# Kernel tuning notes

Measured on AMD Instinct MI355X. Metric: run time of the kernel, lower is better.

Reference implementation:

```python
import jax, jax.numpy as jnp
import numpy as np

K = 3  # kernel size along the folded height sub-dimension

def setup_inputs() -> dict:
    key = jax.random.key(0)
    k1, k2 = jax.random.split(key)
    x = jax.random.normal(k1, (1, 48, 56, 56), dtype=jnp.float32)
    W = jax.random.normal(k2, (192, 48, 3), dtype=jnp.float32)
    return {"x": x, "W": W}

def reference(x, W):
    # x: (1,48,56,56) -> (1,48,8,7,56): split H=56 into (8,7)
    t = x.reshape(1, 48, 8, 7, 56)
    # unfold((3,1), padding=(1,0)) acting on the size-7 axis:
    # pad by 1 on each side, then gather K=3 shifted views.
    tp = jnp.pad(t, ((0, 0), (0, 0), (0, 0), (1, 1), (0, 0)))  # (1,48,8,9,56)
    # patches[l,j,n,k,o,m] = tp[l,j,n,o+k,m], o in [0,7), k in [0,3)
    patches = jnp.stack([tp[:, :, :, k:k + 7, :] for k in range(K)], axis=3)  # (1,48,8,3,7,56)
    # einsum 'ljnkom, ijk -> linom' with W (192,48,3)
    out = jnp.einsum('ljnkom,ijk->linom', patches, W)  # (1,192,8,7,56)
    return out.reshape(1, 192, 56, 56)
```

## Files before the change

kernel.cpp:

```cpp
#include <hip/hip_runtime.h>


#define CH_IN 48
#define CH_OUT 192
#define HW 56
#define SP 3136
#define OB 7
#define M4 14
#define COLS 112
#define SEGS 16
#define JSEG (CH_IN / SEGS)
#define BCOL 16
#define CG 7

__device__ __forceinline__ void fma4(float4& a, float s, const float4& b) {
    a.x += s * b.x; a.y += s * b.y; a.z += s * b.z; a.w += s * b.w;
}
__device__ __forceinline__ void add4(float4& a, const float4& b) {
    a.x += b.x; a.y += b.y; a.z += b.z; a.w += b.w;
}

__global__ __launch_bounds__(256) void conv_split16_kernel(const float* __restrict__ x,
                                                           const float* __restrict__ W,
                                                           float* __restrict__ out) {
    __shared__ float4 lds[SEGS][OB][BCOL];

    const int c   = threadIdx.x & (BCOL - 1);
    const int seg = threadIdx.x >> 4;
    const int i   = blockIdx.x / CG;
    const int cg  = blockIdx.x % CG;

    const int col = cg * BCOL + c;
    const int n   = col / M4;
    const int m4  = col % M4;

    const float* xcol = x + seg * (JSEG * SP) + n * (OB * HW) + m4 * 4;
    const float* wrow = W + i * (CH_IN * 3) + seg * (JSEG * 3);

    float4 acc[OB];
#pragma unroll
    for (int o = 0; o < OB; ++o) acc[o] = make_float4(0.f, 0.f, 0.f, 0.f);

#pragma unroll
    for (int j = 0; j < JSEG; ++j) {
        const float w0 = wrow[j * 3 + 0];
        const float w1 = wrow[j * 3 + 1];
        const float w2 = wrow[j * 3 + 2];

        const float* xj = xcol + j * SP;
        float4 xv[OB];
#pragma unroll
        for (int o = 0; o < OB; ++o)
            xv[o] = *reinterpret_cast<const float4*>(xj + o * HW);

#pragma unroll
        for (int o = 0; o < OB; ++o) {
            if (o > 0)      fma4(acc[o], w0, xv[o - 1]);
            fma4(acc[o], w1, xv[o]);
            if (o < OB - 1) fma4(acc[o], w2, xv[o + 1]);
        }
    }

#pragma unroll
    for (int o = 0; o < OB; ++o) lds[seg][o][c] = acc[o];
    __syncthreads();

    const int t = threadIdx.x;
    if (t < OB * BCOL) {
        const int o  = t >> 4;
        const int cc = t & (BCOL - 1);
        float4 s = lds[0][o][cc];
#pragma unroll
        for (int sgi = 1; sgi < SEGS; ++sgi) add4(s, lds[sgi][o][cc]);

        const int col2 = cg * BCOL + cc;
        const int n2   = col2 / M4;
        const int m42  = col2 % M4;
        *reinterpret_cast<float4*>(out + i * SP + n2 * (OB * HW) + o * HW + m42 * 4) = s;
    }
}

extern "C" void kernel_launch(void* const* d_in, const int* in_sizes, int n_in,
                              void* d_out, int out_size, void* d_ws, size_t ws_size,
                              hipStream_t stream) {
    const float* x = (const float*)d_in[0];
    const float* W = (const float*)d_in[1];
    float* out = (float*)d_out;

    const int grid = CH_OUT * CG;
    conv_split16_kernel<<<grid, 256, 0, stream>>>(x, W, out);
}
```

Baseline: 62.83 us.

## Compute four output channels per block to reuse loaded input tiles

Each block now computes four output channels from the same loaded x values, with 128 threads over 8 column groups. This cuts redundant global loads of x across output channels and shrinks the grid by a factor of two. The cross-segment reduction now runs in two passes through padded shared memory. In exchange, each thread holds 28 float4 accumulators, which raises register pressure, and there are fewer threads per block.

```diff
diff --git a/kernel.cpp b/kernel.cpp
--- a/kernel.cpp
+++ b/kernel.cpp
@@ -9,9 +9,11 @@
 #define M4 14
 #define COLS 112
 #define SEGS 16
-#define JSEG (CH_IN / SEGS)
-#define BCOL 16
-#define CG 7
+#define JSEG 3
+#define BCOL 8
+#define IG 4
+#define CG 14
+#define WST 144
 
 __device__ __forceinline__ void fma4(float4& a, float s, const float4& b) {
     a.x += s * b.x; a.y += s * b.y; a.z += s * b.z; a.w += s * b.w;
@@ -20,33 +22,33 @@
     a.x += b.x; a.y += b.y; a.z += b.z; a.w += b.w;
 }
 
-__global__ __launch_bounds__(256) void conv_split16_kernel(const float* __restrict__ x,
-                                                           const float* __restrict__ W,
-                                                           float* __restrict__ out) {
-    __shared__ float4 lds[SEGS][OB][BCOL];
+__global__ __launch_bounds__(128, 2) void conv_ig4_kernel(const float* __restrict__ x,
+                                                          const float* __restrict__ W,
+                                                          float* __restrict__ out) {
+    __shared__ float4 red[SEGS][2][OB][BCOL + 1];
 
-    const int c   = threadIdx.x & (BCOL - 1);
-    const int seg = threadIdx.x >> 4;
-    const int i   = blockIdx.x / CG;
+    const int tid = threadIdx.x;
+    const int c   = tid & (BCOL - 1);
+    const int seg = tid >> 3;
+    const int ig4 = blockIdx.x / CG;
     const int cg  = blockIdx.x % CG;
+    const int i0  = ig4 * IG;
 
     const int col = cg * BCOL + c;
     const int n   = col / M4;
     const int m4  = col % M4;
 
-    const float* xcol = x + seg * (JSEG * SP) + n * (OB * HW) + m4 * 4;
-    const float* wrow = W + i * (CH_IN * 3) + seg * (JSEG * 3);
+    const float* xcol  = x + seg * (JSEG * SP) + n * (OB * HW) + m4 * 4;
+    const float* wbase = W + i0 * WST + seg * (JSEG * 3);
 
-    float4 acc[OB];
+    float4 acc[IG][OB];
 #pragma unroll
-    for (int o = 0; o < OB; ++o) acc[o] = make_float4(0.f, 0.f, 0.f, 0.f);
+    for (int ig = 0; ig < IG; ++ig)
+#pragma unroll
+        for (int o = 0; o < OB; ++o) acc[ig][o] = make_float4(0.f, 0.f, 0.f, 0.f);
 
 #pragma unroll
     for (int j = 0; j < JSEG; ++j) {
-        const float w0 = wrow[j * 3 + 0];
-        const float w1 = wrow[j * 3 + 1];
-        const float w2 = wrow[j * 3 + 2];
-
         const float* xj = xcol + j * SP;
         float4 xv[OB];
 #pragma unroll
@@ -54,29 +56,44 @@
             xv[o] = *reinterpret_cast<const float4*>(xj + o * HW);
 
 #pragma unroll
-        for (int o = 0; o < OB; ++o) {
-            if (o > 0)      fma4(acc[o], w0, xv[o - 1]);
-            fma4(acc[o], w1, xv[o]);
-            if (o < OB - 1) fma4(acc[o], w2, xv[o + 1]);
+        for (int ig = 0; ig < IG; ++ig) {
+            const float* wp = wbase + ig * WST + j * 3;
+            const float w0 = wp[0];
+            const float w1 = wp[1];
+            const float w2 = wp[2];
+#pragma unroll
+            for (int o = 0; o < OB; ++o) {
+                if (o > 0)      fma4(acc[ig][o], w0, xv[o - 1]);
+                fma4(acc[ig][o], w1, xv[o]);
+                if (o < OB - 1) fma4(acc[ig][o], w2, xv[o + 1]);
+            }
         }
     }
 
 #pragma unroll
-    for (int o = 0; o < OB; ++o) lds[seg][o][c] = acc[o];
-    __syncthreads();
+    for (int p = 0; p < 2; ++p) {
+        __syncthreads();
+#pragma unroll
+        for (int d = 0; d < 2; ++d)
+#pragma unroll
+            for (int o = 0; o < OB; ++o)
+                red[seg][d][o][c] = acc[2 * p + d][o];
+        __syncthreads();
 
-    const int t = threadIdx.x;
-    if (t < OB * BCOL) {
-        const int o  = t >> 4;
-        const int cc = t & (BCOL - 1);
-        float4 s = lds[0][o][cc];
+        if (tid < 2 * OB * BCOL) {
+            const int d  = tid / (OB * BCOL);
+            const int r  = tid % (OB * BCOL);
+            const int o  = r / BCOL;
+            const int cc = r % BCOL;
+            float4 s = red[0][d][o][cc];
 #pragma unroll
-        for (int sgi = 1; sgi < SEGS; ++sgi) add4(s, lds[sgi][o][cc]);
+            for (int sg = 1; sg < SEGS; ++sg) add4(s, red[sg][d][o][cc]);
 
-        const int col2 = cg * BCOL + cc;
-        const int n2   = col2 / M4;
-        const int m42  = col2 % M4;
-        *reinterpret_cast<float4*>(out + i * SP + n2 * (OB * HW) + o * HW + m42 * 4) = s;
+            const int col2 = cg * BCOL + cc;
+            const int n2   = col2 / M4;
+            const int m42  = col2 % M4;
+            *reinterpret_cast<float4*>(out + (i0 + 2 * p + d) * SP + n2 * (OB * HW) + o * HW + m42 * 4) = s;
+        }
     }
 }
 
@@ -87,6 +104,6 @@
     const float* W = (const float*)d_in[1];
     float* out = (float*)d_out;
 
-    const int grid = CH_OUT * CG;
-    conv_split16_kernel<<<grid, 256, 0, stream>>>(x, W, out);
+    const int grid = (CH_OUT / IG) * CG;
+    conv_ig4_kernel<<<grid, 128, 0, stream>>>(x, W, out);
 }
```

Result: faster. 60.70 us (-3.4%).
